# Performance work log

Hardware: AMD Instinct MI355X
Metric: run time of the kernel (lower is better)

## Reference

```python
import jax, jax.numpy as jnp
import numpy as np

D_MODEL = 1024
N_HEADS = 16
HEAD_DIM = D_MODEL // N_HEADS
B, S = 4, 2048


def setup_inputs() -> dict:
    key = jax.random.key(0)
    ks = jax.random.split(key, 12)
    scale = 1.0 / np.sqrt(D_MODEL)
    inp = {
        "query": jax.random.normal(ks[0], (B, S, D_MODEL), dtype=jnp.float32),
        "key": jax.random.normal(ks[1], (B, S, D_MODEL), dtype=jnp.float32),
        "value": jax.random.normal(ks[2], (B, S, D_MODEL), dtype=jnp.float32),
        "mask": jnp.ones((B, 1, S), dtype=jnp.int32),
        "Wq": jax.random.normal(ks[3], (D_MODEL, D_MODEL), dtype=jnp.float32) * scale,
        "bq": jnp.zeros((D_MODEL,), dtype=jnp.float32),
        "Wk": jax.random.normal(ks[4], (D_MODEL, D_MODEL), dtype=jnp.float32) * scale,
        "bk": jnp.zeros((D_MODEL,), dtype=jnp.float32),
        "Wv": jax.random.normal(ks[5], (D_MODEL, D_MODEL), dtype=jnp.float32) * scale,
        "bv": jnp.zeros((D_MODEL,), dtype=jnp.float32),
        "Wo": jax.random.normal(ks[6], (D_MODEL, D_MODEL), dtype=jnp.float32) * scale,
        "bo": jnp.zeros((D_MODEL,), dtype=jnp.float32),
    }
    return inp


def reference(query, key, value, mask, Wq, bq, Wk, bk, Wv, bv, Wo, bo):
    bsz = query.shape[0]
    # Linear projections (torch nn.Linear: x @ W.T + b), split into heads -> [b, h, s, d]
    def proj(x, W, b):
        y = jnp.einsum("bse,de->bsd", x, W) + b
        return y.reshape(bsz, -1, N_HEADS, HEAD_DIM).transpose(0, 2, 1, 3)

    q = proj(query, Wq, bq)
    k = proj(key, Wk, bk)
    v = proj(value, Wv, bv)

    # NOTE: faithful to source — scale by 1/sqrt(d_model), not 1/sqrt(head_dim)
    scores = jnp.einsum("bhqd,bhkd->bhqk", q, k) / jnp.sqrt(jnp.asarray(D_MODEL, q.dtype))
    # mask [b, 1, s_k] -> unsqueeze(1) -> [b, 1, 1, s_k]; fill -inf where mask == 0
    m = mask[:, None, :, :]
    scores = jnp.where(m == 0, jnp.asarray(-jnp.inf, scores.dtype), scores)
    p_attn = jax.nn.softmax(scores, axis=-1)
    ctx = jnp.einsum("bhqk,bhkd->bhqd", p_attn, v)

    concat = ctx.transpose(0, 2, 1, 3).reshape(bsz, -1, D_MODEL)
    out = jnp.einsum("bse,de->bsd", concat, Wo) + bo
    return out
```

## Files before the change

### kernel.cpp

```cpp
#include <hip/hip_runtime.h>
#include <hip/hip_bf16.h>

typedef unsigned short u16;
typedef __attribute__((ext_vector_type(4))) short short4v;
typedef __attribute__((ext_vector_type(8))) short short8;
typedef __attribute__((ext_vector_type(4))) float float4v;

__device__ __forceinline__ void async_copy16(const void* g, void* l) {
  __builtin_amdgcn_global_load_lds(
      (const __attribute__((address_space(1))) unsigned int*)g,
      (__attribute__((address_space(3))) unsigned int*)l,
      16, 0, 0);
}

__device__ __forceinline__ u16 f2bf(float f) {
  __hip_bfloat16 h = __float2bfloat16(f);
  return *reinterpret_cast<u16*>(&h);
}

__device__ __forceinline__ unsigned pack2(float a, float b) {
  return (unsigned)f2bf(a) | ((unsigned)f2bf(b) << 16);
}

struct CArgs {
  const float* in[7];
  u16* out[7];
  int n[7];
};

__global__ void conv_bf16(CArgs a) {
  int t = blockIdx.y;
  int n = a.n[t];
  long i = ((long)blockIdx.x * blockDim.x + threadIdx.x) * 8;
  if (i >= n) return;
  const float4v* f = (const float4v*)(a.in[t] + i);
  float4v lo = f[0], hi = f[1];
  u16 o[8];
  o[0] = f2bf(lo.x); o[1] = f2bf(lo.y); o[2] = f2bf(lo.z); o[3] = f2bf(lo.w);
  o[4] = f2bf(hi.x); o[5] = f2bf(hi.y); o[6] = f2bf(hi.z); o[7] = f2bf(hi.w);
  *(short8*)(a.out[t] + i) = *(const short8*)o;
}

template <bool OUT_F32>
__global__ __launch_bounds__(256, 2)
void gemm_bt(const u16* __restrict__ A, const u16* __restrict__ W,
             const float* __restrict__ bias, void* __restrict__ Cp,
             int M, int N, int K, int mode) {
  __shared__ __attribute__((aligned(16))) u16 As[128 * 32];
  __shared__ __attribute__((aligned(16))) u16 Ws[128 * 32];

  const int tid  = threadIdx.x;
  const int lane = tid & 63;
  const int wave = tid >> 6;
  const int ln15 = lane & 15;
  const int quad = lane >> 4;
  const int m0 = blockIdx.y * 128;
  const int n0 = blockIdx.x * 128;
  const int wm = (wave & 1) * 64;
  const int wn = (wave >> 1) * 64;

  float4v acc[4][4];
#pragma unroll
  for (int i = 0; i < 4; i++)
#pragma unroll
    for (int j = 0; j < 4; j++) acc[i][j] = (float4v)0.0f;

  for (int k0 = 0; k0 < K; k0 += 32) {
#pragma unroll
    for (int c = 0; c < 2; c++) {
      int e = (c * 256 + tid) * 8;
      int r = e >> 5, col = e & 31;
      async_copy16(A + (size_t)(m0 + r) * K + k0 + col, (void*)(As + e));
      async_copy16(W + (size_t)(n0 + r) * K + k0 + col, (void*)(Ws + e));
    }
    __syncthreads();

    short8 af[4], bfr[4];
#pragma unroll
    for (int i = 0; i < 4; i++)
      af[i] = *(const short8*)(As + (wm + i * 16 + ln15) * 32 + quad * 8);
#pragma unroll
    for (int j = 0; j < 4; j++)
      bfr[j] = *(const short8*)(Ws + (wn + j * 16 + ln15) * 32 + quad * 8);
#pragma unroll
    for (int i = 0; i < 4; i++)
#pragma unroll
      for (int j = 0; j < 4; j++)
        acc[i][j] = __builtin_amdgcn_mfma_f32_16x16x32_bf16(af[i], bfr[j], acc[i][j], 0, 0, 0);
    __syncthreads();
  }

#pragma unroll
  for (int j = 0; j < 4; j++) {
    int n = n0 + wn + j * 16 + ln15;
    float bval = bias[n];
#pragma unroll
    for (int i = 0; i < 4; i++) {
#pragma unroll
      for (int r = 0; r < 4; r++) {
        int m = m0 + wm + i * 16 + quad * 4 + r;
        float v = acc[i][j][r] + bval;
        size_t addr;
        if (mode == 0) {
          addr = (size_t)m * N + n;
        } else {
          int b = m >> 11, s = m & 2047;
          int h = n >> 6, dh = n & 63;
          if (mode == 1) addr = (((size_t)(b * 16 + h)) * 2048 + s) * 64 + dh;
          else           addr = (((size_t)(b * 16 + h)) * 64 + dh) * 2048 + s;
        }
        if (OUT_F32) ((float*)Cp)[addr] = v;
        else         ((u16*)Cp)[addr] = f2bf(v);
      }
    }
  }
}

#define SWZ(c, r) ((c) ^ (((r) & 7) << 3))
__global__ __launch_bounds__(256, 3)
void attn(const u16* __restrict__ Q, const u16* __restrict__ K,
          const u16* __restrict__ Vt, const int* __restrict__ mask,
          u16* __restrict__ Ct) {
  __shared__ __attribute__((aligned(16))) u16 Ks[2][64 * 64];
  __shared__ __attribute__((aligned(16))) u16 Vs[2][64 * 64];

  const int tid  = threadIdx.x;
  const int lane = tid & 63;
  const int wave = tid >> 6;
  const int ln15 = lane & 15;
  const int quad = lane >> 4;
  const int bh = blockIdx.y;
  const int b = bh >> 4, h = bh & 15;
  const int q0 = blockIdx.x * 128;
  const int qr0 = wave * 32;

  const u16* Qg = Q + ((size_t)bh * 2048 + q0 + qr0) * 64;
  const u16* Kg = K + (size_t)bh * 2048 * 64;
  const u16* Vg = Vt + (size_t)bh * 64 * 2048;
  const int* mg = mask + b * 2048;

  short8 qf[2][2];
#pragma unroll
  for (int i = 0; i < 2; i++)
#pragma unroll
    for (int kx = 0; kx < 2; kx++)
      qf[i][kx] = *(const short8*)(Qg + (size_t)(i * 16 + ln15) * 64 + kx * 32 + quad * 8);

#pragma unroll
  for (int c = 0; c < 2; c++) {
    int e = (c * 256 + tid) * 8;
    int r = e >> 6, col = e & 63;
    int sc = SWZ(col, r);
    *(short8*)(Ks[0] + r * 64 + sc) = *(const short8*)(Kg + (size_t)r * 64 + col);
    *(short8*)(Vs[0] + r * 64 + sc) = *(const short8*)(Vg + (size_t)r * 2048 + col);
  }

  float4v acc[4][2];
#pragma unroll
  for (int jd = 0; jd < 4; jd++)
#pragma unroll
    for (int i = 0; i < 2; i++) acc[jd][i] = (float4v)0.0f;
  float lrow[2] = {0.0f, 0.0f};

  for (int t = 0; t < 32; t++) {
    const int buf = t & 1;
    __syncthreads();

    short8 kreg[2], vreg[2];
    const bool havenext = (t + 1) < 32;
    if (havenext) {
      int kt2 = (t + 1) * 64;
#pragma unroll
      for (int c = 0; c < 2; c++) {
        int e = (c * 256 + tid) * 8;
        int r = e >> 6, col = e & 63;
        kreg[c] = *(const short8*)(Kg + (size_t)(kt2 + r) * 64 + col);
        vreg[c] = *(const short8*)(Vg + (size_t)r * 2048 + kt2 + col);
      }
    }

    unsigned pk[2][4][2];
#pragma unroll
    for (int j = 0; j < 4; j++) {
      const int krow = j * 16 + ln15;
      short8 kf0 = *(const short8*)(Ks[buf] + krow * 64 + SWZ(quad * 8, krow));
      short8 kf1 = *(const short8*)(Ks[buf] + krow * 64 + SWZ(32 + quad * 8, krow));
      float4v s0 = (float4v)0.0f, s1 = (float4v)0.0f;
      s0 = __builtin_amdgcn_mfma_f32_16x16x32_bf16(kf0, qf[0][0], s0, 0, 0, 0);
      s0 = __builtin_amdgcn_mfma_f32_16x16x32_bf16(kf1, qf[0][1], s0, 0, 0, 0);
      s1 = __builtin_amdgcn_mfma_f32_16x16x32_bf16(kf0, qf[1][0], s1, 0, 0, 0);
      s1 = __builtin_amdgcn_mfma_f32_16x16x32_bf16(kf1, qf[1][1], s1, 0, 0, 0);
      int4 m4 = *(const int4*)(mg + t * 64 + j * 16 + quad * 4);
      float mb0 = (m4.x == 0) ? -1e30f : 0.0f;
      float mb1 = (m4.y == 0) ? -1e30f : 0.0f;
      float mb2 = (m4.z == 0) ? -1e30f : 0.0f;
      float mb3 = (m4.w == 0) ? -1e30f : 0.0f;
      float p00 = __expf(s0[0] * 0.03125f + mb0);
      float p01 = __expf(s0[1] * 0.03125f + mb1);
      float p02 = __expf(s0[2] * 0.03125f + mb2);
      float p03 = __expf(s0[3] * 0.03125f + mb3);
      float p10 = __expf(s1[0] * 0.03125f + mb0);
      float p11 = __expf(s1[1] * 0.03125f + mb1);
      float p12 = __expf(s1[2] * 0.03125f + mb2);
      float p13 = __expf(s1[3] * 0.03125f + mb3);
      lrow[0] += (p00 + p01) + (p02 + p03);
      lrow[1] += (p10 + p11) + (p12 + p13);
      pk[0][j][0] = pack2(p00, p01); pk[0][j][1] = pack2(p02, p03);
      pk[1][j][0] = pack2(p10, p11); pk[1][j][1] = pack2(p12, p13);
    }

    if (havenext) {
#pragma unroll
      for (int c = 0; c < 2; c++) {
        int e = (c * 256 + tid) * 8;
        int r = e >> 6, col = e & 63;
        int sc = SWZ(col, r);
        *(short8*)(Ks[buf ^ 1] + r * 64 + sc) = kreg[c];
        *(short8*)(Vs[buf ^ 1] + r * 64 + sc) = vreg[c];
      }
    }

#pragma unroll
    for (int kx = 0; kx < 2; kx++) {
      const int j0 = kx * 2, j1 = j0 + 1;
      short8 bp[2];
#pragma unroll
      for (int i = 0; i < 2; i++) {
        unsigned t16[2], t32[2], t48[2];
#pragma unroll
        for (int w = 0; w < 2; w++) {
          unsigned vlo = (quad < 2) ? pk[i][j0][w] : pk[i][j1][w];
          unsigned vhi = (quad < 2) ? pk[i][j1][w] : pk[i][j0][w];
          t16[w] = (unsigned)__shfl_xor((int)vlo, 16);
          t32[w] = (unsigned)__shfl_xor((int)vhi, 32);
          t48[w] = (unsigned)__shfl_xor((int)vhi, 48);
        }
        union { unsigned w4[4]; short8 s8; } u;
        u.w4[0] = (quad == 0) ? pk[i][j0][0] : (quad == 1) ? t48[0] : (quad == 2) ? t32[0] : t16[0];
        u.w4[1] = (quad == 0) ? pk[i][j0][1] : (quad == 1) ? t48[1] : (quad == 2) ? t32[1] : t16[1];
        u.w4[2] = (quad == 0) ? t16[0] : (quad == 1) ? t32[0] : (quad == 2) ? t48[0] : pk[i][j1][0];
        u.w4[3] = (quad == 0) ? t16[1] : (quad == 1) ? t32[1] : (quad == 2) ? t48[1] : pk[i][j1][1];
        bp[i] = u.s8;
      }
#pragma unroll
      for (int jd = 0; jd < 4; jd++) {
        const int vrow = jd * 16 + ln15;
        short8 vf = *(const short8*)(Vs[buf] + vrow * 64 + SWZ(kx * 32 + quad * 8, vrow));
#pragma unroll
        for (int i = 0; i < 2; i++)
          acc[jd][i] = __builtin_amdgcn_mfma_f32_16x16x32_bf16(vf, bp[i], acc[jd][i], 0, 0, 0);
      }
    }
  }

#pragma unroll
  for (int i = 0; i < 2; i++) {
    float l = lrow[i];
    l += __shfl_xor(l, 16);
    l += __shfl_xor(l, 32);
    float inv = 1.0f / l;
    int s = q0 + qr0 + i * 16 + ln15;
    u16* base = Ct + ((size_t)(b * 2048 + s)) * 1024 + h * 64 + quad * 4;
#pragma unroll
    for (int jd = 0; jd < 4; jd++) {
      u16 o[4];
      o[0] = f2bf(acc[jd][i][0] * inv);
      o[1] = f2bf(acc[jd][i][1] * inv);
      o[2] = f2bf(acc[jd][i][2] * inv);
      o[3] = f2bf(acc[jd][i][3] * inv);
      *(short4v*)(base + jd * 16) = *(const short4v*)o;
    }
  }
}


extern "C" void kernel_launch(void* const* d_in, const int* in_sizes, int n_in,
                              void* d_out, int out_size, void* d_ws, size_t ws_size,
                              hipStream_t stream) {
  int iq, ik, iv, im, iWq, ibq, iWk, ibk, iWv, ibv, iWo, ibo;
  if (in_sizes[0] == 8388608) {
    iq = 0; ik = 1; iv = 2; im = 3;
    iWq = 4; ibq = 5; iWk = 6; ibk = 7; iWv = 8; ibv = 9; iWo = 10; ibo = 11;
  } else {
    iWk = 0; iWo = 1; iWq = 2; iWv = 3;
    ibk = 4; ibo = 5; ibq = 6; ibv = 7;
    ik = 8; im = 9; iq = 10; iv = 11;
  }
  const float* query = (const float*)d_in[iq];
  const float* key   = (const float*)d_in[ik];
  const float* value = (const float*)d_in[iv];
  const int*   mask  = (const int*)d_in[im];
  const float* Wq = (const float*)d_in[iWq];
  const float* bq = (const float*)d_in[ibq];
  const float* Wk = (const float*)d_in[iWk];
  const float* bk = (const float*)d_in[ibk];
  const float* Wv = (const float*)d_in[iWv];
  const float* bv = (const float*)d_in[ibv];
  const float* Wo = (const float*)d_in[iWo];
  const float* bo = (const float*)d_in[ibo];

  const long U  = 8388608;
  const long Wn = 1048576;
  u16* ws = (u16*)d_ws;
  u16* cq   = ws;
  u16* ck   = cq + U;
  u16* cv   = ck + U;
  u16* cWq  = cv + U;
  u16* cWk  = cWq + Wn;
  u16* cWv  = cWk + Wn;
  u16* cWo  = cWv + Wn;
  u16* qws  = cWo + Wn;
  u16* kws  = qws + U;
  u16* vtws = cq;
  u16* cws  = ck;

  dim3 blk(256);

  CArgs ca;
  ca.in[0] = query; ca.out[0] = cq;  ca.n[0] = (int)U;
  ca.in[1] = key;   ca.out[1] = ck;  ca.n[1] = (int)U;
  ca.in[2] = value; ca.out[2] = cv;  ca.n[2] = (int)U;
  ca.in[3] = Wq;    ca.out[3] = cWq; ca.n[3] = (int)Wn;
  ca.in[4] = Wk;    ca.out[4] = cWk; ca.n[4] = (int)Wn;
  ca.in[5] = Wv;    ca.out[5] = cWv; ca.n[5] = (int)Wn;
  ca.in[6] = Wo;    ca.out[6] = cWo; ca.n[6] = (int)Wn;
  conv_bf16<<<dim3(4096, 7), blk, 0, stream>>>(ca);

  dim3 gproj(8, 64);
  gemm_bt<false><<<gproj, blk, 0, stream>>>(cq, cWq, bq, qws, 8192, 1024, 1024, 1);
  gemm_bt<false><<<gproj, blk, 0, stream>>>(ck, cWk, bk, kws, 8192, 1024, 1024, 1);
  gemm_bt<false><<<gproj, blk, 0, stream>>>(cv, cWv, bv, vtws, 8192, 1024, 1024, 2);
  attn<<<dim3(16, 64), blk, 0, stream>>>(qws, kws, vtws, mask, cws);
  gemm_bt<true><<<gproj, blk, 0, stream>>>(cws, cWo, bo, d_out, 8192, 1024, 1024, 0);
}
```

Measured before the change: 448.1 us.

## Use 32x32 MFMA with permlane32 swap in attention; batch QKV projections

The attention kernel moves from 16x16x32 MFMA tiles to 32x32x16 tiles. Each wave now covers 32 query rows with one f32x16 score block per 32-key chunk, and the P operand is rearranged with permlane32_swap instead of three xor shuffles plus selects. Separately, the Q/K/V projection GEMMs are merged into one launch over a z-dimension of three when the workspace is large enough. That needs an extra V buffer so V no longer aliases the converted query input. The goal is fewer shuffles and instructions per tile, plus a fuller grid and fewer launches; the larger MFMA tile may raise register pressure and affect occupancy.

```diff
diff --git a/kernel.cpp b/kernel.cpp
--- a/kernel.cpp
+++ b/kernel.cpp
@@ -5,6 +5,7 @@
 typedef __attribute__((ext_vector_type(4))) short short4v;
 typedef __attribute__((ext_vector_type(8))) short short8;
 typedef __attribute__((ext_vector_type(4))) float float4v;
+typedef __attribute__((ext_vector_type(16))) float f32x16;
 
 __device__ __forceinline__ void async_copy16(const void* g, void* l) {
   __builtin_amdgcn_global_load_lds(
@@ -42,10 +43,10 @@
 }
 
 template <bool OUT_F32>
-__global__ __launch_bounds__(256, 2)
-void gemm_bt(const u16* __restrict__ A, const u16* __restrict__ W,
-             const float* __restrict__ bias, void* __restrict__ Cp,
-             int M, int N, int K, int mode) {
+__device__ __forceinline__
+void gemm_body(const u16* __restrict__ A, const u16* __restrict__ W,
+               const float* __restrict__ bias, void* __restrict__ Cp,
+               int M, int N, int K, int mode) {
   __shared__ __attribute__((aligned(16))) u16 As[128 * 32];
   __shared__ __attribute__((aligned(16))) u16 Ws[128 * 32];
 
@@ -116,6 +117,25 @@
   }
 }
 
+template <bool OUT_F32>
+__global__ __launch_bounds__(256, 2)
+void gemm_bt(const u16* __restrict__ A, const u16* __restrict__ W,
+             const float* __restrict__ bias, void* __restrict__ Cp,
+             int M, int N, int K, int mode) {
+  gemm_body<OUT_F32>(A, W, bias, Cp, M, N, K, mode);
+}
+
+struct G3 {
+  const u16* A[3]; const u16* W[3]; const float* bias[3];
+  void* C[3]; int mode[3];
+};
+
+__global__ __launch_bounds__(256, 2)
+void gemm_qkv(G3 g) {
+  const int z = blockIdx.z;
+  gemm_body<false>(g.A[z], g.W[z], g.bias[z], g.C[z], 8192, 1024, 1024, g.mode[z]);
+}
+
 #define SWZ(c, r) ((c) ^ (((r) & 7) << 3))
 __global__ __launch_bounds__(256, 3)
 void attn(const u16* __restrict__ Q, const u16* __restrict__ K,
@@ -127,8 +147,8 @@
   const int tid  = threadIdx.x;
   const int lane = tid & 63;
   const int wave = tid >> 6;
-  const int ln15 = lane & 15;
-  const int quad = lane >> 4;
+  const int ln31 = lane & 31;
+  const int hi   = lane >> 5;
   const int bh = blockIdx.y;
   const int b = bh >> 4, h = bh & 15;
   const int q0 = blockIdx.x * 128;
@@ -139,12 +159,10 @@
   const u16* Vg = Vt + (size_t)bh * 64 * 2048;
   const int* mg = mask + b * 2048;
 
-  short8 qf[2][2];
-#pragma unroll
-  for (int i = 0; i < 2; i++)
-#pragma unroll
-    for (int kx = 0; kx < 2; kx++)
-      qf[i][kx] = *(const short8*)(Qg + (size_t)(i * 16 + ln15) * 64 + kx * 32 + quad * 8);
+  short8 qf[4];
+#pragma unroll
+  for (int m = 0; m < 4; m++)
+    qf[m] = *(const short8*)(Qg + (size_t)ln31 * 64 + m * 16 + hi * 8);
 
 #pragma unroll
   for (int c = 0; c < 2; c++) {
@@ -155,12 +173,10 @@
     *(short8*)(Vs[0] + r * 64 + sc) = *(const short8*)(Vg + (size_t)r * 2048 + col);
   }
 
-  float4v acc[4][2];
-#pragma unroll
-  for (int jd = 0; jd < 4; jd++)
-#pragma unroll
-    for (int i = 0; i < 2; i++) acc[jd][i] = (float4v)0.0f;
-  float lrow[2] = {0.0f, 0.0f};
+  f32x16 acc[2];
+#pragma unroll
+  for (int d = 0; d < 2; d++) acc[d] = (f32x16)0.0f;
+  float lrow = 0.0f;
 
   for (int t = 0; t < 32; t++) {
     const int buf = t & 1;
@@ -179,34 +195,41 @@
       }
     }
 
-    unsigned pk[2][4][2];
-#pragma unroll
-    for (int j = 0; j < 4; j++) {
-      const int krow = j * 16 + ln15;
-      short8 kf0 = *(const short8*)(Ks[buf] + krow * 64 + SWZ(quad * 8, krow));
-      short8 kf1 = *(const short8*)(Ks[buf] + krow * 64 + SWZ(32 + quad * 8, krow));
-      float4v s0 = (float4v)0.0f, s1 = (float4v)0.0f;
-      s0 = __builtin_amdgcn_mfma_f32_16x16x32_bf16(kf0, qf[0][0], s0, 0, 0, 0);
-      s0 = __builtin_amdgcn_mfma_f32_16x16x32_bf16(kf1, qf[0][1], s0, 0, 0, 0);
-      s1 = __builtin_amdgcn_mfma_f32_16x16x32_bf16(kf0, qf[1][0], s1, 0, 0, 0);
-      s1 = __builtin_amdgcn_mfma_f32_16x16x32_bf16(kf1, qf[1][1], s1, 0, 0, 0);
-      int4 m4 = *(const int4*)(mg + t * 64 + j * 16 + quad * 4);
-      float mb0 = (m4.x == 0) ? -1e30f : 0.0f;
-      float mb1 = (m4.y == 0) ? -1e30f : 0.0f;
-      float mb2 = (m4.z == 0) ? -1e30f : 0.0f;
-      float mb3 = (m4.w == 0) ? -1e30f : 0.0f;
-      float p00 = __expf(s0[0] * 0.03125f + mb0);
-      float p01 = __expf(s0[1] * 0.03125f + mb1);
-      float p02 = __expf(s0[2] * 0.03125f + mb2);
-      float p03 = __expf(s0[3] * 0.03125f + mb3);
-      float p10 = __expf(s1[0] * 0.03125f + mb0);
-      float p11 = __expf(s1[1] * 0.03125f + mb1);
-      float p12 = __expf(s1[2] * 0.03125f + mb2);
-      float p13 = __expf(s1[3] * 0.03125f + mb3);
-      lrow[0] += (p00 + p01) + (p02 + p03);
-      lrow[1] += (p10 + p11) + (p12 + p13);
-      pk[0][j][0] = pack2(p00, p01); pk[0][j][1] = pack2(p02, p03);
-      pk[1][j][0] = pack2(p10, p11); pk[1][j][1] = pack2(p12, p13);
+    unsigned bw[2][2][4];
+#pragma unroll
+    for (int kb = 0; kb < 2; kb++) {
+      f32x16 s = (f32x16)0.0f;
+#pragma unroll
+      for (int m = 0; m < 4; m++) {
+        const int krow = kb * 32 + ln31;
+        short8 kf = *(const short8*)(Ks[buf] + krow * 64 + SWZ(m * 16 + hi * 8, krow));
+        s = __builtin_amdgcn_mfma_f32_32x32x16_bf16(kf, qf[m], s, 0, 0, 0);
+      }
+      unsigned w[8];
+#pragma unroll
+      for (int g = 0; g < 4; g++) {
+        int4 m4 = *(const int4*)(mg + t * 64 + kb * 32 + g * 8 + hi * 4);
+        float mb0 = (m4.x == 0) ? -1e30f : 0.0f;
+        float mb1 = (m4.y == 0) ? -1e30f : 0.0f;
+        float mb2 = (m4.z == 0) ? -1e30f : 0.0f;
+        float mb3 = (m4.w == 0) ? -1e30f : 0.0f;
+        float p0 = __expf(s[4 * g + 0] * 0.03125f + mb0);
+        float p1 = __expf(s[4 * g + 1] * 0.03125f + mb1);
+        float p2 = __expf(s[4 * g + 2] * 0.03125f + mb2);
+        float p3 = __expf(s[4 * g + 3] * 0.03125f + mb3);
+        lrow += (p0 + p1) + (p2 + p3);
+        w[2 * g]     = pack2(p0, p1);
+        w[2 * g + 1] = pack2(p2, p3);
+      }
+#pragma unroll
+      for (int c = 0; c < 2; c++) {
+        auto r0 = __builtin_amdgcn_permlane32_swap(w[c], w[2 + c], false, false);
+        bw[kb][0][c]     = r0[0];
+        bw[kb][0][2 + c] = r0[1];
+        auto r1 = __builtin_amdgcn_permlane32_swap(w[4 + c], w[6 + c], false, false);
+        bw[kb][1][c]     = r1[0];
+        bw[kb][1][2 + c] = r1[1];
+      }
     }
 
     if (havenext) {
@@ -221,54 +244,37 @@
     }
 
 #pragma unroll
-    for (int kx = 0; kx < 2; kx++) {
-      const int j0 = kx * 2, j1 = j0 + 1;
-      short8 bp[2];
-#pragma unroll
-      for (int i = 0; i < 2; i++) {
-        unsigned t16[2], t32[2], t48[2];
-#pragma unroll
-        for (int w = 0; w < 2; w++) {
-          unsigned vlo = (quad < 2) ? pk[i][j0][w] : pk[i][j1][w];
-          unsigned vhi = (quad < 2) ? pk[i][j1][w] : pk[i][j0][w];
-          t16[w] = (unsigned)__shfl_xor((int)vlo, 16);
-          t32[w] = (unsigned)__shfl_xor((int)vhi, 32);
-          t48[w] = (unsigned)__shfl_xor((int)vhi, 48);
+    for (int d = 0; d < 2; d++) {
+#pragma unroll
+      for (int kb = 0; kb < 2; kb++) {
+#pragma unroll
+        for (int mp = 0; mp < 2; mp++) {
+          const int vrow = d * 32 + ln31;
+          short8 vf = *(const short8*)(Vs[buf] + vrow * 64 +
+                                       SWZ(kb * 32 + mp * 16 + hi * 8, vrow));
+          union { unsigned w4[4]; short8 s8; } u;
+          u.w4[0] = bw[kb][mp][0]; u.w4[1] = bw[kb][mp][1];
+          u.w4[2] = bw[kb][mp][2]; u.w4[3] = bw[kb][mp][3];
+          acc[d] = __builtin_amdgcn_mfma_f32_32x32x16_bf16(vf, u.s8, acc[d], 0, 0, 0);
         }
-        union { unsigned w4[4]; short8 s8; } u;
-        u.w4[0] = (quad == 0) ? pk[i][j0][0] : (quad == 1) ? t48[0] : (quad == 2) ? t32[0] : t16[0];
-        u.w4[1] = (quad == 0) ? pk[i][j0][1] : (quad == 1) ? t48[1] : (quad == 2) ? t32[1] : t16[1];
-        u.w4[2] = (quad == 0) ? t16[0] : (quad == 1) ? t32[0] : (quad == 2) ? t48[0] : pk[i][j1][0];
-        u.w4[3] = (quad == 0) ? t16[1] : (quad == 1) ? t32[1] : (quad == 2) ? t48[1] : pk[i][j1][1];
-        bp[i] = u.s8;
-      }
-#pragma unroll
-      for (int jd = 0; jd < 4; jd++) {
-        const int vrow = jd * 16 + ln15;
-        short8 vf = *(const short8*)(Vs[buf] + vrow * 64 + SWZ(kx * 32 + quad * 8, vrow));
-#pragma unroll
-        for (int i = 0; i < 2; i++)
-          acc[jd][i] = __builtin_amdgcn_mfma_f32_16x16x32_bf16(vf, bp[i], acc[jd][i], 0, 0, 0);
-      }
-    }
-  }
-
-#pragma unroll
-  for (int i = 0; i < 2; i++) {
-    float l = lrow[i];
-    l += __shfl_xor(l, 16);
-    l += __shfl_xor(l, 32);
-    float inv = 1.0f / l;
-    int s = q0 + qr0 + i * 16 + ln15;
-    u16* base = Ct + ((size_t)(b * 2048 + s)) * 1024 + h * 64 + quad * 4;
-#pragma unroll
-    for (int jd = 0; jd < 4; jd++) {
+      }
+    }
+  }
+
+  float l = lrow + __shfl_xor(lrow, 32);
+  float inv = 1.0f / l;
+  const int s = q0 + qr0 + ln31;
+  u16* base = Ct + ((size_t)(b * 2048 + s)) * 1024 + h * 64 + hi * 4;
+#pragma unroll
+  for (int d = 0; d < 2; d++) {
+#pragma unroll
+    for (int g = 0; g < 4; g++) {
       u16 o[4];
-      o[0] = f2bf(acc[jd][i][0] * inv);
-      o[1] = f2bf(acc[jd][i][1] * inv);
-      o[2] = f2bf(acc[jd][i][2] * inv);
-      o[3] = f2bf(acc[jd][i][3] * inv);
-      *(short4v*)(base + jd * 16) = *(const short4v*)o;
+      o[0] = f2bf(acc[d][4 * g + 0] * inv);
+      o[1] = f2bf(acc[d][4 * g + 1] * inv);
+      o[2] = f2bf(acc[d][4 * g + 2] * inv);
+      o[3] = f2bf(acc[d][4 * g + 3] * inv);
+      *(short4v*)(base + d * 32 + g * 8) = *(const short4v*)o;
     }
   }
 }
@@ -311,8 +317,11 @@
   u16* cWo  = cWv + Wn;
   u16* qws  = cWo + Wn;
   u16* kws  = qws + U;
-  u16* vtws = cq;
   u16* cws  = ck;
+
+  const size_t need_batched = (size_t)(7 * U + 4 * Wn) * sizeof(u16);
+  const bool batched = ws_size >= need_batched;
+  u16* vtws = batched ? (kws + U) : cq;
 
   dim3 blk(256);
 
@@ -327,9 +336,17 @@
   conv_bf16<<<dim3(4096, 7), blk, 0, stream>>>(ca);
 
   dim3 gproj(8, 64);
-  gemm_bt<false><<<gproj, blk, 0, stream>>>(cq, cWq, bq, qws, 8192, 1024, 1024, 1);
-  gemm_bt<false><<<gproj, blk, 0, stream>>>(ck, cWk, bk, kws, 8192, 1024, 1024, 1);
-  gemm_bt<false><<<gproj, blk, 0, stream>>>(cv, cWv, bv, vtws, 8192, 1024, 1024, 2);
+  if (batched) {
+    G3 g3;
+    g3.A[0] = cq; g3.W[0] = cWq; g3.bias[0] = bq; g3.C[0] = qws;  g3.mode[0] = 1;
+    g3.A[1] = ck; g3.W[1] = cWk; g3.bias[1] = bk; g3.C[1] = kws;  g3.mode[1] = 1;
+    g3.A[2] = cv; g3.W[2] = cWv; g3.bias[2] = bv; g3.C[2] = vtws; g3.mode[2] = 2;
+    gemm_qkv<<<dim3(8, 64, 3), blk, 0, stream>>>(g3);
+  } else {
+    gemm_bt<false><<<gproj, blk, 0, stream>>>(cq, cWq, bq, qws, 8192, 1024, 1024, 1);
+    gemm_bt<false><<<gproj, blk, 0, stream>>>(ck, cWk, bk, kws, 8192, 1024, 1024, 1);
+    gemm_bt<false><<<gproj, blk, 0, stream>>>(cv, cWv, bv, vtws, 8192, 1024, 1024, 2);
+  }
   attn<<<dim3(16, 64), blk, 0, stream>>>(qws, kws, vtws, mask, cws);
   gemm_bt<true><<<gproj, blk, 0, stream>>>(cws, cWo, bo, d_out, 8192, 1024, 1024, 0);
 }
```

Measured after the change: 437.2 us. 1.02x faster.
